# Optimization experiments

Hardware: AMD Instinct MI355X
Metric: run time of the kernel (lower is better)

Reference implementation:

```python
import jax, jax.numpy as jnp
import numpy as np
from functools import partial

B, C, H, W = 32, 16, 256, 256
HIDDEN = 128
N_FILT = 3

SOBEL_X = jnp.array([[-1., 0., 1.], [-2., 0., 2.], [-1., 0., 1.]], dtype=jnp.float32)
SOBEL_Y = jnp.array([[-1., -2., -1.], [0., 0., 0.], [1., 2., 1.]], dtype=jnp.float32)
CELL_ID = jnp.array([[0., 0., 0.], [0., 1., 0.], [0., 0., 0.]], dtype=jnp.float32)
ALIVE_K = jnp.ones((1, 1, 3, 3), dtype=jnp.float32)


def _conv3x3_same(x, kernel):
    # x: [B, Cin, H, W], kernel: [Cout, Cin, 3, 3], padding=1
    return jax.lax.conv_general_dilated(
        x, kernel, window_strides=(1, 1), padding='SAME',
        dimension_numbers=('NCHW', 'OIHW', 'NCHW'))


def _perceive(x, k2d):
    # Original weight is k2d repeated to [16,16,3,3] (identical kernel for every
    # in/out channel pair), so conv2d(x, W) == conv2d(sum_c x_c, k2d) broadcast
    # to 16 identical output channels. Same math, far less work.
    xs = jnp.sum(x, axis=1, keepdims=True)            # [B,1,H,W]
    out = _conv3x3_same(xs, k2d[None, None, :, :])     # [B,1,H,W]
    return jnp.broadcast_to(out, (x.shape[0], C, x.shape[2], x.shape[3]))


def setup_inputs() -> dict:
    key = jax.random.key(0)
    k1, k2, k3 = jax.random.split(key, 3)
    x = jax.random.uniform(k1, (B, C, H, W), dtype=jnp.float32)
    random_mask = jax.random.randint(k2, (B, 1, H, W), 0, 2, dtype=jnp.int32)
    w1 = jax.random.normal(k3, (HIDDEN, N_FILT * C), dtype=jnp.float32) * 0.05
    b1 = jnp.zeros((HIDDEN,), dtype=jnp.float32)
    # NOTE: original inits fc2.weight to zeros; use small random so dx is nontrivial
    w2 = jax.random.normal(jax.random.fold_in(key, 7), (C, HIDDEN), dtype=jnp.float32) * 0.05
    b2 = jnp.zeros((C,), dtype=jnp.float32)
    return {'x': x, 'random_mask': random_mask, 'w1': w1, 'b1': b1, 'w2': w2, 'b2': b2}


def reference(x, random_mask, w1, b1, w2, b2):
    # perception: [sobelX, sobelY, cellId] blocks of 16 channels each -> [B,48,H,W]
    perception = jnp.concatenate(
        [_perceive(x, SOBEL_X), _perceive(x, SOBEL_Y), _perceive(x, CELL_ID)], axis=1)
    # 1x1 conv MLP
    h = jnp.einsum('oc,bchw->bohw', w1, perception) + b1[None, :, None, None]
    h = jax.nn.relu(h)
    dx = jnp.einsum('oc,bchw->bohw', w2, h) + b2[None, :, None, None]
    # stochastic update: mask broadcast over all 16 channels
    x_new = x + dx * random_mask.astype(x.dtype)
    # alive mask: 3x3 ones conv over (alpha > 0.1), then > 0, broadcast over channels
    alpha_alive = (x_new[:, 3:4, :, :] > 0.1).astype(x.dtype)  # [B,1,H,W]
    alive = _conv3x3_same(alpha_alive, ALIVE_K) > 0.0           # [B,1,H,W] bool
    return x_new * alive.astype(x.dtype)
```

## Files before the change

### kernel.cpp

```cpp
#include <hip/hip_runtime.h>
#include <hip/hip_bf16.h>

#define B_   32
#define C_   16
#define H_   256
#define W_   256
#define HW_  65536
#define HID_ 128
#define T_   8
#define NBLK_ (B_*H_/T_)

typedef __attribute__((ext_vector_type(8))) short bf16x8;
typedef __attribute__((ext_vector_type(4))) float f32x4;

__device__ __forceinline__ short f2bf(float f) {
    __hip_bfloat16 h = __float2bfloat16(f);
    return __builtin_bit_cast(short, h);
}

__device__ __forceinline__ int cvt_pk_bf16(float lo, float hi) {
    int r;
    asm("v_cvt_pk_bf16_f32 %0, %1, %2" : "=v"(r) : "v"(lo), "v"(hi));
    return r;
}

__global__ __launch_bounds__(128) void nca_prep(
    const float* __restrict__ w1, const float* __restrict__ b1,
    float4* __restrict__ coef4)
{
    int o = threadIdx.x;
    float A = 0.f, Bc = 0.f, Cc = 0.f;
    #pragma unroll
    for (int k = 0;  k < 16; ++k) A  += w1[o*48 + k];
    #pragma unroll
    for (int k = 16; k < 32; ++k) Bc += w1[o*48 + k];
    #pragma unroll
    for (int k = 32; k < 48; ++k) Cc += w1[o*48 + k];
    coef4[o] = make_float4(A, Bc, Cc, b1[o]);
}

__global__ __launch_bounds__(256, 4) void nca_fused(
    const float* __restrict__ x, const int* __restrict__ mask,
    const float4* __restrict__ coef4, const float* __restrict__ w2,
    const float* __restrict__ b2,
    float* __restrict__ out, unsigned char* __restrict__ alpha)
{
    __shared__ float srow[T_+2][W_];
    __shared__ short hlds[4*2048];

    const int tid  = threadIdx.x;
    const int lane = tid & 63;
    const int widx = tid >> 6;
    const int col  = tid;
    const int q = lane & 15;
    const int g = lane >> 4;

    const int blk = blockIdx.x;
    const int b   = blk >> 5;
    const int r0  = (blk & 31) * T_;

    const float* xb = x    + (size_t)b * C_ * HW_;
    const int*   mb = mask + (size_t)b * HW_;
    float*       ob = (float*)out + (size_t)b * C_ * HW_;
    unsigned char* ab = alpha + (size_t)b * HW_;

    bf16x8 afrag[4];
    #pragma unroll
    for (int kb = 0; kb < 4; ++kb) {
        const float* wp = w2 + q*HID_ + kb*32 + g*8;
        bf16x8 a;
        #pragma unroll
        for (int j = 0; j < 8; ++j) a[j] = f2bf(wp[j]);
        afrag[kb] = a;
    }
    f32x4 bias;
    #pragma unroll
    for (int r = 0; r < 4; ++r) bias[r] = b2[g*4 + r];

    const int wswz = (lane ^ (lane >> 2)) & 3;
    const int rsw  = (q ^ (q >> 2)) & 3;
    short* hw  = hlds + widx*2048;
    char*  hwb = (char*)hw;

    float xnext[C_];
    {
        float s0 = 0.f;
        if (r0 > 0) {
            #pragma unroll
            for (int c = 0; c < C_; ++c)
                s0 += xb[(size_t)c*HW_ + (size_t)(r0-1)*W_ + col];
        }
        float s1 = 0.f;
        #pragma unroll
        for (int c = 0; c < C_; ++c)
            s1 += xb[(size_t)c*HW_ + (size_t)r0*W_ + col];
        #pragma unroll
        for (int c = 0; c < C_; ++c)
            xnext[c] = xb[(size_t)c*HW_ + (size_t)(r0+1)*W_ + col];
        srow[0][col] = s0;
        srow[1][col] = s1;
    }

    for (int r = 0; r < T_; ++r) {
        const int row = r0 + r;

        {
            float s = 0.f;
            #pragma unroll
            for (int c = 0; c < C_; ++c) s += xnext[c];
            srow[r+2][col] = s;
        }
        __syncthreads();

        if (r < T_-1) {
            const int nr = r0 + r + 2;
            if (nr < H_) {
                #pragma unroll
                for (int c = 0; c < C_; ++c)
                    xnext[c] = xb[(size_t)c*HW_ + (size_t)nr*W_ + col];
            } else {
                #pragma unroll
                for (int c = 0; c < C_; ++c) xnext[c] = 0.f;
            }
        }

        const bool jm = col > 0, jp = col < W_-1;
        const float* sA = srow[r];
        const float* sB = srow[r+1];
        const float* sC = srow[r+2];
        float n00 = jm ? sA[col-1] : 0.f, n01 = sA[col], n02 = jp ? sA[col+1] : 0.f;
        float n10 = jm ? sB[col-1] : 0.f, n11 = sB[col], n12 = jp ? sB[col+1] : 0.f;
        float n20 = jm ? sC[col-1] : 0.f, n21 = sC[col], n22 = jp ? sC[col+1] : 0.f;
        float px = (n02 - n00) + 2.f*(n12 - n10) + (n22 - n20);
        float py = (n20 - n00) + 2.f*(n21 - n01) + (n22 - n02);
        float sc = n11;

        f32x4 acc[4];
        #pragma unroll
        for (int t = 0; t < 4; ++t) acc[t] = bias;

        #pragma unroll
        for (int kb = 0; kb < 4; ++kb) {
            #pragma unroll
            for (int c = 0; c < 4; ++c) {
                float h[8];
                #pragma unroll
                for (int u = 0; u < 8; ++u) {
                    const float4 cf = coef4[kb*32 + c*8 + u];
                    h[u] = fmaxf(fmaf(cf.x, px, fmaf(cf.y, py, fmaf(cf.z, sc, cf.w))), 0.f);
                }
                int4 hd = make_int4(cvt_pk_bf16(h[0], h[1]), cvt_pk_bf16(h[2], h[3]),
                                    cvt_pk_bf16(h[4], h[5]), cvt_pk_bf16(h[6], h[7]));
                *(int4*)(hw + lane*32 + ((c ^ wswz) << 3)) = hd;
            }
            __builtin_amdgcn_wave_barrier();
            #pragma unroll
            for (int t = 0; t < 4; ++t) {
                const int pp = t*16 + q;
                bf16x8 bfrag = *(const bf16x8*)(hw + pp*32 + (((g ^ rsw) & 3) << 3));
                acc[t] = __builtin_amdgcn_mfma_f32_16x16x32_bf16(
                             afrag[kb], bfrag, acc[t], 0, 0, 0);
            }
            __builtin_amdgcn_wave_barrier();
        }

        #pragma unroll
        for (int t = 0; t < 4; ++t) {
            const int pp = t*16 + q;
            *(f32x4*)(hwb + pp*64 + ((g ^ (pp & 3)) << 4)) = acc[t];
        }
        __builtin_amdgcn_wave_barrier();

        const float m = (float)mb[row*W_ + col];
        float xn3 = 0.f;
        #pragma unroll
        for (int u = 0; u < 4; ++u) {
            f32x4 a = *(const f32x4*)(hwb + lane*64 + ((u ^ (lane & 3)) << 4));
            #pragma unroll
            for (int e = 0; e < 4; ++e) {
                const int ch = u*4 + e;
                float xv = xb[(size_t)ch*HW_ + (size_t)row*W_ + col];
                float xn = fmaf(a[e], m, xv);
                ob[(size_t)ch*HW_ + (size_t)row*W_ + col] = xn;
                if (ch == 3) xn3 = xn;
            }
        }
        ab[row*W_ + col] = (xn3 > 0.1f) ? (unsigned char)1 : (unsigned char)0;
        __builtin_amdgcn_wave_barrier();
    }
}

__global__ __launch_bounds__(256) void nca_alive(
    const unsigned char* __restrict__ alpha, float* __restrict__ out)
{
    int t = blockIdx.x * blockDim.x + threadIdx.x;
    if (t >= B_*HW_) return;
    int b = t >> 16;
    int p = t & (HW_-1);
    int i = p >> 8;
    int j = p & (W_-1);
    const unsigned char* ab = alpha + (size_t)b * HW_;

    bool im = i > 0, ip = i < H_-1, jm = j > 0, jp = j < W_-1;
    int acc = ab[p];
    acc += jm ? ab[p-1] : 0;
    acc += jp ? ab[p+1] : 0;
    if (im) {
        acc += ab[p-W_];
        acc += jm ? ab[p-W_-1] : 0;
        acc += jp ? ab[p-W_+1] : 0;
    }
    if (ip) {
        acc += ab[p+W_];
        acc += jm ? ab[p+W_-1] : 0;
        acc += jp ? ab[p+W_+1] : 0;
    }
    if (acc == 0) {
        size_t base = (size_t)b * C_ * HW_ + p;
        #pragma unroll
        for (int c = 0; c < C_; ++c) out[base + (size_t)c * HW_] = 0.f;
    }
}

extern "C" void kernel_launch(void* const* d_in, const int* in_sizes, int n_in,
                              void* d_out, int out_size, void* d_ws, size_t ws_size,
                              hipStream_t stream)
{
    const float* x    = (const float*)d_in[0];
    const int*   mask = (const int*)d_in[1];
    const float* w1   = (const float*)d_in[2];
    const float* b1   = (const float*)d_in[3];
    const float* w2   = (const float*)d_in[4];
    const float* b2   = (const float*)d_in[5];
    float* out = (float*)d_out;

    char* ws = (char*)d_ws;
    unsigned char* alpha = (unsigned char*)ws;
    float4*        coef4 = (float4*)(ws + (size_t)B_*HW_);

    nca_prep<<<1, 128, 0, stream>>>(w1, b1, coef4);

    nca_fused<<<NBLK_, 256, 0, stream>>>(x, mask, coef4, w2, b2, out, alpha);

    int n = B_*HW_;
    nca_alive<<<(n + 255)/256, 256, 0, stream>>>(alpha, out);
}
```

Before: 91.17 us.

## Halve row tile, move w2 fragments to LDS, write outputs directly from MFMA layout

The row tile per block drops from 8 to 4, which doubles the block count. The w2 A-fragments are staged once in LDS and reloaded per k-block instead of being held in registers, which cuts register pressure. The epilogue no longer round-trips the accumulators through LDS: each lane reads x and writes out directly in the MFMA output layout, and the mask values are loaded per strip. Index math also moves from size_t to 32-bit ints. The trade-offs are more recomputed halo rows, strided 16-wide global accesses per channel group in place of full-row coalesced ones, and only a quarter of the lanes writing alpha.

```diff
diff --git a/kernel.cpp b/kernel.cpp
--- a/kernel.cpp
+++ b/kernel.cpp
@@ -7,7 +7,7 @@
 #define W_   256
 #define HW_  65536
 #define HID_ 128
-#define T_   8
+#define T_   4
 #define NBLK_ (B_*H_/T_)
 
 typedef __attribute__((ext_vector_type(8))) short bf16x8;
@@ -47,6 +47,7 @@
 {
     __shared__ float srow[T_+2][W_];
     __shared__ short hlds[4*2048];
+    __shared__ short w2lds[4*64*8];
 
     const int tid  = threadIdx.x;
     const int lane = tid & 63;
@@ -56,31 +57,31 @@
     const int g = lane >> 4;
 
     const int blk = blockIdx.x;
-    const int b   = blk >> 5;
-    const int r0  = (blk & 31) * T_;
+    const int b   = blk >> 6;
+    const int r0  = (blk & 63) * T_;
 
     const float* xb = x    + (size_t)b * C_ * HW_;
     const int*   mb = mask + (size_t)b * HW_;
     float*       ob = (float*)out + (size_t)b * C_ * HW_;
     unsigned char* ab = alpha + (size_t)b * HW_;
 
-    bf16x8 afrag[4];
-    #pragma unroll
-    for (int kb = 0; kb < 4; ++kb) {
-        const float* wp = w2 + q*HID_ + kb*32 + g*8;
+    {
+        const int kb = tid >> 6, l = tid & 63;
+        const int qq = l & 15, gg = l >> 4;
+        const float* wp = w2 + qq*HID_ + kb*32 + gg*8;
         bf16x8 a;
         #pragma unroll
         for (int j = 0; j < 8; ++j) a[j] = f2bf(wp[j]);
-        afrag[kb] = a;
-    }
+        *(bf16x8*)(w2lds + tid*8) = a;
+    }
+
     f32x4 bias;
     #pragma unroll
     for (int r = 0; r < 4; ++r) bias[r] = b2[g*4 + r];
 
     const int wswz = (lane ^ (lane >> 2)) & 3;
     const int rsw  = (q ^ (q >> 2)) & 3;
-    short* hw  = hlds + widx*2048;
-    char*  hwb = (char*)hw;
+    short* hw = hlds + widx*2048;
 
     float xnext[C_];
     {
@@ -88,15 +89,15 @@
         if (r0 > 0) {
             #pragma unroll
             for (int c = 0; c < C_; ++c)
-                s0 += xb[(size_t)c*HW_ + (size_t)(r0-1)*W_ + col];
+                s0 += xb[c*HW_ + (r0-1)*W_ + col];
         }
         float s1 = 0.f;
         #pragma unroll
         for (int c = 0; c < C_; ++c)
-            s1 += xb[(size_t)c*HW_ + (size_t)r0*W_ + col];
+            s1 += xb[c*HW_ + r0*W_ + col];
         #pragma unroll
         for (int c = 0; c < C_; ++c)
-            xnext[c] = xb[(size_t)c*HW_ + (size_t)(r0+1)*W_ + col];
+            xnext[c] = xb[c*HW_ + (r0+1)*W_ + col];
         srow[0][col] = s0;
         srow[1][col] = s1;
     }
@@ -117,12 +118,18 @@
             if (nr < H_) {
                 #pragma unroll
                 for (int c = 0; c < C_; ++c)
-                    xnext[c] = xb[(size_t)c*HW_ + (size_t)nr*W_ + col];
+                    xnext[c] = xb[c*HW_ + nr*W_ + col];
             } else {
                 #pragma unroll
                 for (int c = 0; c < C_; ++c) xnext[c] = 0.f;
             }
         }
+
+        const int pstrip = row*W_ + (widx << 6);
+        float mv[4];
+        #pragma unroll
+        for (int t = 0; t < 4; ++t)
+            mv[t] = (float)mb[pstrip + t*16 + q];
 
         const bool jm = col > 0, jp = col < W_-1;
         const float* sA = srow[r];
@@ -154,39 +161,32 @@
                 *(int4*)(hw + lane*32 + ((c ^ wswz) << 3)) = hd;
             }
             __builtin_amdgcn_wave_barrier();
+            bf16x8 af = *(const bf16x8*)(w2lds + (kb*64 + lane)*8);
             #pragma unroll
             for (int t = 0; t < 4; ++t) {
                 const int pp = t*16 + q;
                 bf16x8 bfrag = *(const bf16x8*)(hw + pp*32 + (((g ^ rsw) & 3) << 3));
                 acc[t] = __builtin_amdgcn_mfma_f32_16x16x32_bf16(
-                             afrag[kb], bfrag, acc[t], 0, 0, 0);
+                             af, bfrag, acc[t], 0, 0, 0);
             }
             __builtin_amdgcn_wave_barrier();
         }
 
         #pragma unroll
         for (int t = 0; t < 4; ++t) {
-            const int pp = t*16 + q;
-            *(f32x4*)(hwb + pp*64 + ((g ^ (pp & 3)) << 4)) = acc[t];
-        }
-        __builtin_amdgcn_wave_barrier();
-
-        const float m = (float)mb[row*W_ + col];
-        float xn3 = 0.f;
-        #pragma unroll
-        for (int u = 0; u < 4; ++u) {
-            f32x4 a = *(const f32x4*)(hwb + lane*64 + ((u ^ (lane & 3)) << 4));
+            const int pp = pstrip + t*16 + q;
+            float xn3 = 0.f;
             #pragma unroll
             for (int e = 0; e < 4; ++e) {
-                const int ch = u*4 + e;
-                float xv = xb[(size_t)ch*HW_ + (size_t)row*W_ + col];
-                float xn = fmaf(a[e], m, xv);
-                ob[(size_t)ch*HW_ + (size_t)row*W_ + col] = xn;
+                const int ch = g*4 + e;
+                float xv = xb[ch*HW_ + pp];
+                float xn = fmaf(acc[t][e], mv[t], xv);
+                ob[ch*HW_ + pp] = xn;
                 if (ch == 3) xn3 = xn;
             }
-        }
-        ab[row*W_ + col] = (xn3 > 0.1f) ? (unsigned char)1 : (unsigned char)0;
-        __builtin_amdgcn_wave_barrier();
+            if (g == 0) ab[pp] = (xn3 > 0.1f) ? (unsigned char)1
+                                              : (unsigned char)0;
+        }
     }
 }
 
```

Measured after the change: 97.58 us. +7.0%, slower.
